# Kernel optimization log

Measured on AMD Instinct MI355X. Metric: run time of the kernel, lower is better.

## Reference

```python
import jax, jax.numpy as jnp
import numpy as np

EMB_SCALE = 0.001  # embedding_scale when normalize=False


def setup_inputs() -> dict:
    key = jax.random.key(0)
    k1, k2 = jax.random.split(key)
    N, S, C, V, K = 8, 4096, 2, 128, 512
    x0 = jax.random.normal(k1, (N, S, C, V), dtype=jnp.float32)
    embedding = jax.random.normal(k2, (C, K, V), dtype=jnp.float32) * EMB_SCALE
    return {"x0": x0, "embedding": embedding}


def reference(x0, embedding):
    # normalize=False path: x = x0, embedding used as-is
    N, S, C, V = x0.shape
    K = embedding.shape[1]
    x = x0
    xf = x.reshape(N * S, C, V)  # (B, C, V), B = N*S tokens

    # (the ||x||^2 term is constant over k). Avoids materializing (B, C, K, V).
    dots = jnp.einsum('bcv,ckv->bck', xf, embedding)          # (B, C, K)
    e_sq = jnp.sum(embedding * embedding, axis=2)             # (C, K)
    dist2 = e_sq[None, :, :] - 2.0 * dots                     # (B, C, K)
    index = jnp.argmin(dist2, axis=2)                         # (B, C) int

    # Entropy of codebook usage (original divides by len(index) == B rows)
    B = N * S
    hist = jnp.bincount(index.reshape(-1), length=K).astype(jnp.float32)
    prob = hist / jnp.float32(B)
    entropy = -jnp.sum(jnp.where(hist > 0, prob * jnp.log(jnp.maximum(prob, 1e-30)), 0.0))

    # Gather: output[b, c] = embedding[c, index[b, c]]
    output = embedding[jnp.arange(C), index]                  # (B, C, V)
    output = output.reshape(N, S, C, V)

    out0 = jax.lax.stop_gradient(output - x) + x              # straight-through
    out1 = jnp.sum((jax.lax.stop_gradient(x) - output) ** 2, axis=3)  # (N,S,C)
    out2 = (jnp.sum((x - jax.lax.stop_gradient(output)) ** 2, axis=3)
            + jnp.sum((x - x0) ** 2, axis=3))                 # (N,S,C); (x-x0)==0 here
    return (out0, out1, out2, entropy)
```

## Files before the change

kernel.cpp:

```cpp
#include <hip/hip_runtime.h>
#include <math.h>

#define N_TOK    32768
#define C_CH     2
#define V_DIM    128
#define K_CODES  512
#define TPB      64
#define WCAP     128
#define BAND     4.0e-3f

typedef short     bf16v8 __attribute__((ext_vector_type(8)));
typedef float     f32x4  __attribute__((ext_vector_type(4)));
typedef unsigned  u32x4  __attribute__((ext_vector_type(4)));

__device__ inline unsigned f2bf(float f) {
    unsigned u = __float_as_uint(f);
    return (u + 0x7FFFu + ((u >> 16) & 1u)) >> 16;
}
__device__ inline unsigned mapf(float d) {
    unsigned u = __float_as_uint(d);
    return ((int)u < 0) ? ~u : (u | 0x80000000u);
}
__device__ inline float unmapf(unsigned u) {
    return __uint_as_float((u & 0x80000000u) ? (u & 0x7FFFFFFFu) : ~u);
}

__global__ __launch_bounds__(64) void vq_prep(const float* __restrict__ emb,
                                              float* __restrict__ e_sq,
                                              unsigned int* __restrict__ hist,
                                              unsigned char* __restrict__ img) {
    const int row  = blockIdx.x;
    const int lane = threadIdx.x;
    const float a = emb[(size_t)row * V_DIM + lane];
    const float b = emb[(size_t)row * V_DIM + 64 + lane];
    float s = a * a + b * b;
#pragma unroll
    for (int off = 32; off; off >>= 1) s += __shfl_down(s, off);
    if (lane == 0) {
        e_sq[row] = s;
        if (row < K_CODES) hist[row] = 0u;
    }
    if (lane < 16) {
        const float* src = emb + (size_t)row * V_DIM + lane * 8;
        u32x4 val;
#pragma unroll
        for (int q = 0; q < 4; ++q)
            val[q] = f2bf(src[2 * q]) | (f2bf(src[2 * q + 1]) << 16);
        *reinterpret_cast<u32x4*>(img + ((size_t)row * 16 + lane) * 16) = val;
    }
}

__global__ __launch_bounds__(256, 2) void vq_main(const float* __restrict__ x0,
                                                  const float* __restrict__ emb,
                                                  const float* __restrict__ e_sq,
                                                  const unsigned char* __restrict__ img,
                                                  unsigned int* __restrict__ hist,
                                                  float* __restrict__ out0,
                                                  float* __restrict__ out1,
                                                  float* __restrict__ out2) {
    __shared__ float xx_s[TPB];
    __shared__ unsigned int dmin_s[TPB];
    __shared__ unsigned long long best_s[TPB];
    __shared__ unsigned int cand_w[4][WCAP];
    __shared__ int cnt_w[4];

    const int c    = blockIdx.y;
    const int gt0  = blockIdx.x * TPB;
    const int t    = threadIdx.x;
    const int lane = t & 63;
    const int w    = t >> 6;
    const int l15  = lane & 15;
    const int l4   = lane >> 4;

    if (t < TPB) { dmin_s[t] = 0xFFFFFFFFu; best_s[t] = ~0ull; }
    if (t < 4) cnt_w[t] = 0;

    u32x4 Bf[8][4];
    {
        const unsigned char* imgc = img + (size_t)(c * K_CODES + w * 128) * 256;
#pragma unroll
        for (int ct = 0; ct < 8; ++ct)
#pragma unroll
            for (int kk = 0; kk < 4; ++kk)
                Bf[ct][kk] = *reinterpret_cast<const u32x4*>(
                    imgc + (size_t)(ct * 16 + l15) * 256 + (kk * 4 + l4) * 16);
    }
    float esq_r[8];
#pragma unroll
    for (int ct = 0; ct < 8; ++ct)
        esq_r[ct] = e_sq[c * K_CODES + w * 128 + ct * 16 + l15];

    __syncthreads();

    f32x4 raw[8];
    auto LOADX = [&](int tile_) {
        const float* xp = x0 + ((size_t)(gt0 + tile_ * 16 + l15) * C_CH + c) * V_DIM
                        + l4 * 8;
#pragma unroll
        for (int kk = 0; kk < 4; ++kk) {
            raw[2 * kk]     = *reinterpret_cast<const f32x4*>(xp + kk * 32);
            raw[2 * kk + 1] = *reinterpret_cast<const f32x4*>(xp + kk * 32 + 4);
        }
    };

    LOADX(0);
#pragma unroll
    for (int tile = 0; tile < 4; ++tile) {
        u32x4 A[4];
        float part = 0.f;
#pragma unroll
        for (int kk = 0; kk < 4; ++kk) {
            const f32x4 lo = raw[2 * kk], hi = raw[2 * kk + 1];
            u32x4 v;
            v[0] = f2bf(lo[0]) | (f2bf(lo[1]) << 16);
            v[1] = f2bf(lo[2]) | (f2bf(lo[3]) << 16);
            v[2] = f2bf(hi[0]) | (f2bf(hi[1]) << 16);
            v[3] = f2bf(hi[2]) | (f2bf(hi[3]) << 16);
            A[kk] = v;
#pragma unroll
            for (int z = 0; z < 4; ++z) {
                part = fmaf(lo[z], lo[z], part);
                part = fmaf(hi[z], hi[z], part);
            }
        }
        part += __shfl_xor(part, 16);
        part += __shfl_xor(part, 32);
        if (w == 0 && l4 == 0) xx_s[tile * 16 + l15] = part;

        if (tile < 3) LOADX(tile + 1);

        f32x4 acc[8];
#pragma unroll
        for (int ct = 0; ct < 8; ++ct) acc[ct] = (f32x4){0.f, 0.f, 0.f, 0.f};
#pragma unroll
        for (int kk = 0; kk < 4; ++kk)
#pragma unroll
            for (int ct = 0; ct < 8; ++ct)
                acc[ct] = __builtin_amdgcn_mfma_f32_16x16x32_bf16(
                    __builtin_bit_cast(bf16v8, A[kk]),
                    __builtin_bit_cast(bf16v8, Bf[ct][kk]), acc[ct], 0, 0, 0);

#pragma unroll
        for (int ct = 0; ct < 8; ++ct)
#pragma unroll
            for (int r = 0; r < 4; ++r)
                acc[ct][r] = fmaf(-2.f, acc[ct][r], esq_r[ct]);

#pragma unroll
        for (int r = 0; r < 4; ++r) {
            float v = acc[0][r];
#pragma unroll
            for (int ct = 1; ct < 8; ++ct) v = fminf(v, acc[ct][r]);
#pragma unroll
            for (int s = 1; s < 16; s <<= 1) v = fminf(v, __shfl_xor(v, s));
            if (l15 == 0)
                atomicMin(&dmin_s[tile * 16 + l4 * 4 + r], mapf(v));
        }

#pragma unroll
        for (int r = 0; r < 4; ++r) {
            const int tok = tile * 16 + l4 * 4 + r;
            const float thr = unmapf(dmin_s[tok]) + BAND;
#pragma unroll
            for (int ct = 0; ct < 8; ++ct) {
                if (acc[ct][r] <= thr) {
                    const int k = w * 128 + ct * 16 + l15;
                    const int pos = atomicAdd(&cnt_w[w], 1);
                    if (pos < WCAP)
                        cand_w[w][pos] = ((unsigned)tok << 9) | (unsigned)k;
                }
            }
        }
    }

    {
        const int cnt0 = cnt_w[w];
        const int cnt  = cnt0 < WCAP ? cnt0 : WCAP;
        for (int i = l4; i < cnt; i += 4) {
            const unsigned key = cand_w[w][i];
            const int tok = key >> 9;
            const int kc  = key & (K_CODES - 1);
            const float* xg = x0 + ((size_t)(gt0 + tok) * C_CH + c) * V_DIM + l15 * 8;
            const float* eg = emb + ((size_t)c * K_CODES + kc) * V_DIM + l15 * 8;
            const f32x4 xa = *reinterpret_cast<const f32x4*>(xg);
            const f32x4 xb = *reinterpret_cast<const f32x4*>(xg + 4);
            const f32x4 ea = *reinterpret_cast<const f32x4*>(eg);
            const f32x4 eb = *reinterpret_cast<const f32x4*>(eg + 4);
            float d8 = 0.f;
#pragma unroll
            for (int z = 0; z < 4; ++z) {
                d8 = fmaf(xa[z], ea[z], d8);
                d8 = fmaf(xb[z], eb[z], d8);
            }
#pragma unroll
            for (int s = 1; s < 16; s <<= 1) d8 += __shfl_xor(d8, s);
            if (l15 == 0) {
                const float d = fmaf(-2.f, d8, e_sq[c * K_CODES + kc]);
                atomicMin(&best_s[tok],
                          ((unsigned long long)mapf(d) << 32) | (unsigned)kc);
            }
        }
    }
    __syncthreads();

    if (t < TPB) {
        const unsigned long long b = best_s[t];
        const int k = (int)(b & (unsigned)(K_CODES - 1));
        const float d = unmapf((unsigned)(b >> 32));
        const float o12 = xx_s[t] + d;
        const size_t oi = (size_t)(gt0 + t) * C_CH + c;
        out1[oi] = o12;
        out2[oi] = o12;
        atomicAdd(&hist[k], 1u);
    }

#pragma unroll
    for (int p = 0; p < 8; ++p) {
        const int tok = p * 8 + (t >> 5);
        const int v4  = t & 31;
        const int k   = (int)(best_s[tok] & (unsigned long long)(K_CODES - 1));
        const f32x4 ev = *reinterpret_cast<const f32x4*>(
            emb + ((size_t)c * K_CODES + k) * V_DIM + v4 * 4);
        const f32x4 xv = *reinterpret_cast<const f32x4*>(
            x0 + ((size_t)(gt0 + tok) * C_CH + c) * V_DIM + v4 * 4);
        f32x4 ov;
#pragma unroll
        for (int z = 0; z < 4; ++z) ov[z] = (ev[z] - xv[z]) + xv[z];
        *reinterpret_cast<f32x4*>(
            out0 + ((size_t)(gt0 + tok) * C_CH + c) * V_DIM + v4 * 4) = ov;
    }
}

__global__ __launch_bounds__(512) void vq_entropy(const unsigned int* __restrict__ hist,
                                                  float* __restrict__ ent) {
    const int t = threadIdx.x;
    float v = 0.f;
    const unsigned int h = hist[t];
    if (h > 0u) {
        const float p = (float)h * (1.0f / 32768.0f);
        v = p * logf(p);
    }
#pragma unroll
    for (int off = 32; off; off >>= 1) v += __shfl_down(v, off);
    __shared__ float s[8];
    if ((t & 63) == 0) s[t >> 6] = v;
    __syncthreads();
    if (t == 0) {
        float tot = 0.f;
#pragma unroll
        for (int i = 0; i < 8; ++i) tot += s[i];
        ent[0] = -tot;
    }
}

extern "C" void kernel_launch(void* const* d_in, const int* in_sizes, int n_in,
                              void* d_out, int out_size, void* d_ws, size_t ws_size,
                              hipStream_t stream) {
    const float* x0  = (const float*)d_in[0];
    const float* emb = (const float*)d_in[1];

    float*         e_sq = (float*)d_ws;
    unsigned int*  hist = (unsigned int*)((char*)d_ws + 4096);
    unsigned char* img  = (unsigned char*)d_ws + 8192;

    float* out0 = (float*)d_out;
    float* out1 = out0 + (size_t)N_TOK * C_CH * V_DIM;
    float* out2 = out1 + (size_t)N_TOK * C_CH;
    float* ent  = out2 + (size_t)N_TOK * C_CH;

    vq_prep<<<C_CH * K_CODES, 64, 0, stream>>>(emb, e_sq, hist, img);
    vq_main<<<dim3(N_TOK / TPB, C_CH), 256, 0, stream>>>(x0, emb, e_sq, img, hist,
                                                         out0, out1, out2);
    vq_entropy<<<1, K_CODES, 0, stream>>>(hist, ent);
}
```

Measured before the change: 76.49 us.

## Split VQ main kernel into screening and high-occupancy output kernels

Splits the fused kernel in two. The first kernel only screens codebook distances and writes each token's best packed index to a workspace buffer. A new lightweight kernel, running at high occupancy, gathers the chosen code, writes the straight-through output, computes the squared error directly instead of from ||x||^2 plus the distance, and updates the histogram. This takes the epilogue work and the ||x||^2 computation out of the register-heavy MFMA kernel. The cost is an extra launch and re-reading x0 from memory.

```diff
diff --git a/kernel.cpp b/kernel.cpp
--- a/kernel.cpp
+++ b/kernel.cpp
@@ -50,15 +50,11 @@
     }
 }
 
-__global__ __launch_bounds__(256, 2) void vq_main(const float* __restrict__ x0,
-                                                  const float* __restrict__ emb,
-                                                  const float* __restrict__ e_sq,
-                                                  const unsigned char* __restrict__ img,
-                                                  unsigned int* __restrict__ hist,
-                                                  float* __restrict__ out0,
-                                                  float* __restrict__ out1,
-                                                  float* __restrict__ out2) {
-    __shared__ float xx_s[TPB];
+__global__ __launch_bounds__(256, 2) void vq_screen(const float* __restrict__ x0,
+                                                    const float* __restrict__ emb,
+                                                    const float* __restrict__ e_sq,
+                                                    const unsigned char* __restrict__ img,
+                                                    unsigned long long* __restrict__ bestg) {
     __shared__ unsigned int dmin_s[TPB];
     __shared__ unsigned long long best_s[TPB];
     __shared__ unsigned int cand_w[4][WCAP];
@@ -107,7 +103,6 @@
 #pragma unroll
     for (int tile = 0; tile < 4; ++tile) {
         u32x4 A[4];
-        float part = 0.f;
 #pragma unroll
         for (int kk = 0; kk < 4; ++kk) {
             const f32x4 lo = raw[2 * kk], hi = raw[2 * kk + 1];
@@ -117,15 +112,7 @@
             v[2] = f2bf(hi[0]) | (f2bf(hi[1]) << 16);
             v[3] = f2bf(hi[2]) | (f2bf(hi[3]) << 16);
             A[kk] = v;
-#pragma unroll
-            for (int z = 0; z < 4; ++z) {
-                part = fmaf(lo[z], lo[z], part);
-                part = fmaf(hi[z], hi[z], part);
-            }
-        }
-        part += __shfl_xor(part, 16);
-        part += __shfl_xor(part, 32);
-        if (w == 0 && l4 == 0) xx_s[tile * 16 + l15] = part;
+        }
 
         if (tile < 3) LOADX(tile + 1);
 
@@ -145,7 +132,6 @@
 #pragma unroll
             for (int r = 0; r < 4; ++r)
                 acc[ct][r] = fmaf(-2.f, acc[ct][r], esq_r[ct]);
-
 #pragma unroll
         for (int r = 0; r < 4; ++r) {
             float v = acc[0][r];
@@ -203,31 +189,46 @@
     }
     __syncthreads();
 
-    if (t < TPB) {
-        const unsigned long long b = best_s[t];
-        const int k = (int)(b & (unsigned)(K_CODES - 1));
-        const float d = unmapf((unsigned)(b >> 32));
-        const float o12 = xx_s[t] + d;
-        const size_t oi = (size_t)(gt0 + t) * C_CH + c;
-        out1[oi] = o12;
-        out2[oi] = o12;
+    if (t < TPB)
+        bestg[(size_t)(gt0 + t) * C_CH + c] = best_s[t];
+}
+
+__global__ __launch_bounds__(256, 8) void vq_out(const float* __restrict__ x0,
+                                                 const float* __restrict__ emb,
+                                                 const unsigned long long* __restrict__ bestg,
+                                                 unsigned int* __restrict__ hist,
+                                                 float* __restrict__ out0,
+                                                 float* __restrict__ out1,
+                                                 float* __restrict__ out2) {
+    const int t   = threadIdx.x;
+    const int g   = t >> 5;
+    const int gl  = t & 31;
+    const size_t r = (size_t)blockIdx.x * 8 + g;
+    const int c   = (int)(r & 1);
+
+    const unsigned long long b = bestg[r];
+    const int k = (int)(b & (unsigned long long)(K_CODES - 1));
+
+    const f32x4 ev = *reinterpret_cast<const f32x4*>(
+        emb + ((size_t)c * K_CODES + k) * V_DIM + gl * 4);
+    const f32x4 xv = *reinterpret_cast<const f32x4*>(x0 + r * V_DIM + gl * 4);
+
+    f32x4 ov;
+    float s = 0.f;
+#pragma unroll
+    for (int z = 0; z < 4; ++z) {
+        ov[z] = (ev[z] - xv[z]) + xv[z];
+        const float dfz = xv[z] - ev[z];
+        s = fmaf(dfz, dfz, s);
+    }
+    *reinterpret_cast<f32x4*>(out0 + r * V_DIM + gl * 4) = ov;
+
+#pragma unroll
+    for (int m = 1; m <= 16; m <<= 1) s += __shfl_xor(s, m);
+    if (gl == 0) {
+        out1[r] = s;
+        out2[r] = s;
         atomicAdd(&hist[k], 1u);
-    }
-
-#pragma unroll
-    for (int p = 0; p < 8; ++p) {
-        const int tok = p * 8 + (t >> 5);
-        const int v4  = t & 31;
-        const int k   = (int)(best_s[tok] & (unsigned long long)(K_CODES - 1));
-        const f32x4 ev = *reinterpret_cast<const f32x4*>(
-            emb + ((size_t)c * K_CODES + k) * V_DIM + v4 * 4);
-        const f32x4 xv = *reinterpret_cast<const f32x4*>(
-            x0 + ((size_t)(gt0 + tok) * C_CH + c) * V_DIM + v4 * 4);
-        f32x4 ov;
-#pragma unroll
-        for (int z = 0; z < 4; ++z) ov[z] = (ev[z] - xv[z]) + xv[z];
-        *reinterpret_cast<f32x4*>(
-            out0 + ((size_t)(gt0 + tok) * C_CH + c) * V_DIM + v4 * 4) = ov;
     }
 }
 
@@ -259,9 +260,10 @@
     const float* x0  = (const float*)d_in[0];
     const float* emb = (const float*)d_in[1];
 
-    float*         e_sq = (float*)d_ws;
-    unsigned int*  hist = (unsigned int*)((char*)d_ws + 4096);
-    unsigned char* img  = (unsigned char*)d_ws + 8192;
+    float*              e_sq  = (float*)d_ws;
+    unsigned int*       hist  = (unsigned int*)((char*)d_ws + 4096);
+    unsigned char*      img   = (unsigned char*)d_ws + 8192;
+    unsigned long long* bestg = (unsigned long long*)((char*)d_ws + 8192 + 262144);
 
     float* out0 = (float*)d_out;
     float* out1 = out0 + (size_t)N_TOK * C_CH * V_DIM;
@@ -269,7 +271,8 @@
     float* ent  = out2 + (size_t)N_TOK * C_CH;
 
     vq_prep<<<C_CH * K_CODES, 64, 0, stream>>>(emb, e_sq, hist, img);
-    vq_main<<<dim3(N_TOK / TPB, C_CH), 256, 0, stream>>>(x0, emb, e_sq, img, hist,
-                                                         out0, out1, out2);
+    vq_screen<<<dim3(N_TOK / TPB, C_CH), 256, 0, stream>>>(x0, emb, e_sq, img, bestg);
+    vq_out<<<N_TOK * C_CH / 8, 256, 0, stream>>>(x0, emb, bestg, hist,
+                                                 out0, out1, out2);
     vq_entropy<<<1, K_CODES, 0, stream>>>(hist, ent);
 }
```

Measured after the change: 109.1 us. +42.6%, slower.

## Drop fp32 refinement pass, use bf16 argmin directly with 8 waves per block

Applied to the files above, without the earlier changes.

Removes the candidate-band fp32 re-scoring stage and instead takes the argmin straight from the bf16 MFMA distances, packing distance and index into a 64-bit key reduced by shuffles and atomicMin. The block grows to 512 threads, so each wave holds 64 codes instead of 128, halving per-wave register fragments, and inline asm pins the B fragments in registers. out1/out2 are now computed exactly from the gathered code vector in the epilogue. The bf16-only selection can pick a different code than the fp32 reference when distances are nearly tied, which risks correctness.

```diff
diff --git a/kernel.cpp b/kernel.cpp
--- a/kernel.cpp
+++ b/kernel.cpp
@@ -6,8 +6,6 @@
 #define V_DIM    128
 #define K_CODES  512
 #define TPB      64
-#define WCAP     128
-#define BAND     4.0e-3f
 
 typedef short     bf16v8 __attribute__((ext_vector_type(8)));
 typedef float     f32x4  __attribute__((ext_vector_type(4)));
@@ -21,8 +19,11 @@
     unsigned u = __float_as_uint(d);
     return ((int)u < 0) ? ~u : (u | 0x80000000u);
 }
-__device__ inline float unmapf(unsigned u) {
-    return __uint_as_float((u & 0x80000000u) ? (u & 0x7FFFFFFFu) : ~u);
+
+__device__ inline void pin4(u32x4& v) {
+    unsigned a0 = v[0], a1 = v[1], a2 = v[2], a3 = v[3];
+    asm volatile("" : "+v"(a0), "+v"(a1), "+v"(a2), "+v"(a3));
+    v[0] = a0; v[1] = a1; v[2] = a2; v[3] = a3;
 }
 
 __global__ __launch_bounds__(64) void vq_prep(const float* __restrict__ emb,
@@ -50,7 +51,7 @@
     }
 }
 
-__global__ __launch_bounds__(256, 2) void vq_main(const float* __restrict__ x0,
+__global__ __launch_bounds__(512, 2) void vq_main(const float* __restrict__ x0,
                                                   const float* __restrict__ emb,
                                                   const float* __restrict__ e_sq,
                                                   const unsigned char* __restrict__ img,
@@ -58,11 +59,7 @@
                                                   float* __restrict__ out0,
                                                   float* __restrict__ out1,
                                                   float* __restrict__ out2) {
-    __shared__ float xx_s[TPB];
-    __shared__ unsigned int dmin_s[TPB];
     __shared__ unsigned long long best_s[TPB];
-    __shared__ unsigned int cand_w[4][WCAP];
-    __shared__ int cnt_w[4];
 
     const int c    = blockIdx.y;
     const int gt0  = blockIdx.x * TPB;
@@ -72,23 +69,24 @@
     const int l15  = lane & 15;
     const int l4   = lane >> 4;
 
-    if (t < TPB) { dmin_s[t] = 0xFFFFFFFFu; best_s[t] = ~0ull; }
-    if (t < 4) cnt_w[t] = 0;
-
-    u32x4 Bf[8][4];
+    if (t < TPB) best_s[t] = ~0ull;
+
+    u32x4 Bf[4][4];
     {
-        const unsigned char* imgc = img + (size_t)(c * K_CODES + w * 128) * 256;
-#pragma unroll
-        for (int ct = 0; ct < 8; ++ct)
-#pragma unroll
-            for (int kk = 0; kk < 4; ++kk)
+        const unsigned char* imgc = img + (size_t)(c * K_CODES + w * 64) * 256;
+#pragma unroll
+        for (int ct = 0; ct < 4; ++ct)
+#pragma unroll
+            for (int kk = 0; kk < 4; ++kk) {
                 Bf[ct][kk] = *reinterpret_cast<const u32x4*>(
                     imgc + (size_t)(ct * 16 + l15) * 256 + (kk * 4 + l4) * 16);
-    }
-    float esq_r[8];
-#pragma unroll
-    for (int ct = 0; ct < 8; ++ct)
-        esq_r[ct] = e_sq[c * K_CODES + w * 128 + ct * 16 + l15];
+                pin4(Bf[ct][kk]);
+            }
+    }
+    float esq_r[4];
+#pragma unroll
+    for (int ct = 0; ct < 4; ++ct)
+        esq_r[ct] = e_sq[c * K_CODES + w * 64 + ct * 16 + l15];
 
     __syncthreads();
 
@@ -107,7 +105,6 @@
 #pragma unroll
     for (int tile = 0; tile < 4; ++tile) {
         u32x4 A[4];
-        float part = 0.f;
 #pragma unroll
         for (int kk = 0; kk < 4; ++kk) {
             const f32x4 lo = raw[2 * kk], hi = raw[2 * kk + 1];
@@ -117,117 +114,70 @@
             v[2] = f2bf(hi[0]) | (f2bf(hi[1]) << 16);
             v[3] = f2bf(hi[2]) | (f2bf(hi[3]) << 16);
             A[kk] = v;
-#pragma unroll
-            for (int z = 0; z < 4; ++z) {
-                part = fmaf(lo[z], lo[z], part);
-                part = fmaf(hi[z], hi[z], part);
-            }
-        }
-        part += __shfl_xor(part, 16);
-        part += __shfl_xor(part, 32);
-        if (w == 0 && l4 == 0) xx_s[tile * 16 + l15] = part;
+        }
 
         if (tile < 3) LOADX(tile + 1);
 
-        f32x4 acc[8];
-#pragma unroll
-        for (int ct = 0; ct < 8; ++ct) acc[ct] = (f32x4){0.f, 0.f, 0.f, 0.f};
+        f32x4 acc[4];
+#pragma unroll
+        for (int ct = 0; ct < 4; ++ct) acc[ct] = (f32x4){0.f, 0.f, 0.f, 0.f};
 #pragma unroll
         for (int kk = 0; kk < 4; ++kk)
 #pragma unroll
-            for (int ct = 0; ct < 8; ++ct)
+            for (int ct = 0; ct < 4; ++ct)
                 acc[ct] = __builtin_amdgcn_mfma_f32_16x16x32_bf16(
                     __builtin_bit_cast(bf16v8, A[kk]),
                     __builtin_bit_cast(bf16v8, Bf[ct][kk]), acc[ct], 0, 0, 0);
 
 #pragma unroll
-        for (int ct = 0; ct < 8; ++ct)
-#pragma unroll
-            for (int r = 0; r < 4; ++r)
-                acc[ct][r] = fmaf(-2.f, acc[ct][r], esq_r[ct]);
-
-#pragma unroll
         for (int r = 0; r < 4; ++r) {
-            float v = acc[0][r];
-#pragma unroll
-            for (int ct = 1; ct < 8; ++ct) v = fminf(v, acc[ct][r]);
-#pragma unroll
-            for (int s = 1; s < 16; s <<= 1) v = fminf(v, __shfl_xor(v, s));
+            unsigned long long m = ~0ull;
+#pragma unroll
+            for (int ct = 0; ct < 4; ++ct) {
+                const float d = fmaf(-2.f, acc[ct][r], esq_r[ct]);
+                const unsigned long long p =
+                    ((unsigned long long)mapf(d) << 32)
+                    | (unsigned)(w * 64 + ct * 16 + l15);
+                if (p < m) m = p;
+            }
+#pragma unroll
+            for (int s = 1; s < 16; s <<= 1) {
+                const unsigned long long o = __shfl_xor(m, s);
+                if (o < m) m = o;
+            }
             if (l15 == 0)
-                atomicMin(&dmin_s[tile * 16 + l4 * 4 + r], mapf(v));
-        }
-
-#pragma unroll
-        for (int r = 0; r < 4; ++r) {
-            const int tok = tile * 16 + l4 * 4 + r;
-            const float thr = unmapf(dmin_s[tok]) + BAND;
-#pragma unroll
-            for (int ct = 0; ct < 8; ++ct) {
-                if (acc[ct][r] <= thr) {
-                    const int k = w * 128 + ct * 16 + l15;
-                    const int pos = atomicAdd(&cnt_w[w], 1);
-                    if (pos < WCAP)
-                        cand_w[w][pos] = ((unsigned)tok << 9) | (unsigned)k;
-                }
-            }
-        }
-    }
-
-    {
-        const int cnt0 = cnt_w[w];
-        const int cnt  = cnt0 < WCAP ? cnt0 : WCAP;
-        for (int i = l4; i < cnt; i += 4) {
-            const unsigned key = cand_w[w][i];
-            const int tok = key >> 9;
-            const int kc  = key & (K_CODES - 1);
-            const float* xg = x0 + ((size_t)(gt0 + tok) * C_CH + c) * V_DIM + l15 * 8;
-            const float* eg = emb + ((size_t)c * K_CODES + kc) * V_DIM + l15 * 8;
-            const f32x4 xa = *reinterpret_cast<const f32x4*>(xg);
-            const f32x4 xb = *reinterpret_cast<const f32x4*>(xg + 4);
-            const f32x4 ea = *reinterpret_cast<const f32x4*>(eg);
-            const f32x4 eb = *reinterpret_cast<const f32x4*>(eg + 4);
-            float d8 = 0.f;
-#pragma unroll
-            for (int z = 0; z < 4; ++z) {
-                d8 = fmaf(xa[z], ea[z], d8);
-                d8 = fmaf(xb[z], eb[z], d8);
-            }
-#pragma unroll
-            for (int s = 1; s < 16; s <<= 1) d8 += __shfl_xor(d8, s);
-            if (l15 == 0) {
-                const float d = fmaf(-2.f, d8, e_sq[c * K_CODES + kc]);
-                atomicMin(&best_s[tok],
-                          ((unsigned long long)mapf(d) << 32) | (unsigned)kc);
-            }
+                atomicMin(&best_s[tile * 16 + l4 * 4 + r], m);
         }
     }
     __syncthreads();
 
-    if (t < TPB) {
-        const unsigned long long b = best_s[t];
-        const int k = (int)(b & (unsigned)(K_CODES - 1));
-        const float d = unmapf((unsigned)(b >> 32));
-        const float o12 = xx_s[t] + d;
-        const size_t oi = (size_t)(gt0 + t) * C_CH + c;
-        out1[oi] = o12;
-        out2[oi] = o12;
-        atomicAdd(&hist[k], 1u);
-    }
-
-#pragma unroll
-    for (int p = 0; p < 8; ++p) {
-        const int tok = p * 8 + (t >> 5);
-        const int v4  = t & 31;
+    const int g  = t >> 5;
+    const int gl = t & 31;
+#pragma unroll
+    for (int i = 0; i < 4; ++i) {
+        const int tok = i * 16 + g;
         const int k   = (int)(best_s[tok] & (unsigned long long)(K_CODES - 1));
+        const size_t rowi = (size_t)(gt0 + tok) * C_CH + c;
         const f32x4 ev = *reinterpret_cast<const f32x4*>(
-            emb + ((size_t)c * K_CODES + k) * V_DIM + v4 * 4);
+            emb + ((size_t)c * K_CODES + k) * V_DIM + gl * 4);
         const f32x4 xv = *reinterpret_cast<const f32x4*>(
-            x0 + ((size_t)(gt0 + tok) * C_CH + c) * V_DIM + v4 * 4);
+            x0 + rowi * V_DIM + gl * 4);
         f32x4 ov;
-#pragma unroll
-        for (int z = 0; z < 4; ++z) ov[z] = (ev[z] - xv[z]) + xv[z];
-        *reinterpret_cast<f32x4*>(
-            out0 + ((size_t)(gt0 + tok) * C_CH + c) * V_DIM + v4 * 4) = ov;
+        float s = 0.f;
+#pragma unroll
+        for (int z = 0; z < 4; ++z) {
+            ov[z] = (ev[z] - xv[z]) + xv[z];
+            const float dz = xv[z] - ev[z];
+            s = fmaf(dz, dz, s);
+        }
+        *reinterpret_cast<f32x4*>(out0 + rowi * V_DIM + gl * 4) = ov;
+#pragma unroll
+        for (int m2 = 1; m2 <= 16; m2 <<= 1) s += __shfl_xor(s, m2);
+        if (gl == 0) {
+            out1[rowi] = s;
+            out2[rowi] = s;
+            atomicAdd(&hist[k], 1u);
+        }
     }
 }
 
@@ -269,7 +219,7 @@
     float* ent  = out2 + (size_t)N_TOK * C_CH;
 
     vq_prep<<<C_CH * K_CODES, 64, 0, stream>>>(emb, e_sq, hist, img);
-    vq_main<<<dim3(N_TOK / TPB, C_CH), 256, 0, stream>>>(x0, emb, e_sq, img, hist,
+    vq_main<<<dim3(N_TOK / TPB, C_CH), 512, 0, stream>>>(x0, emb, e_sq, img, hist,
                                                          out0, out1, out2);
     vq_entropy<<<1, K_CODES, 0, stream>>>(hist, ent);
 }
```

New measurement: 88.40 us. 1.16x slower.
